# Kernel tuning notes

Measured on AMD Instinct MI355X. Metric: run time of the kernel, lower is better.

The kernel has to match this reference:

```python
import jax, jax.numpy as jnp
import numpy as np

VOCAB_SIZE = 250002
UNUSED_TOKEN_IDS = np.array([0, 2, 1, 3])  # cls, eos, pad, unk (XLM-R tokenizer)
EPS = 1e-12


def _l2norm(x):
    n = jnp.sqrt(jnp.sum(x * x, axis=-1, keepdims=True))
    return x / jnp.maximum(n, EPS)


def setup_inputs() -> dict:
    key = jax.random.key(0)
    k1, k2, k3, k4 = jax.random.split(key, 4)
    B, S, H = 16, 2048, 1024
    hidden_state = jax.random.normal(k1, (B, S, H), dtype=jnp.float32)
    attention_mask = jnp.ones((B, S), dtype=jnp.float32)
    input_ids = jax.random.randint(k2, (B, S), 0, VOCAB_SIZE, dtype=jnp.int64)
    sparse_W = jax.random.normal(k3, (H, 1), dtype=jnp.float32) * 0.02
    sparse_b = jnp.zeros((1,), dtype=jnp.float32)
    colbert_W = jax.random.normal(k4, (H, H), dtype=jnp.float32) * 0.02
    colbert_b = jnp.zeros((H,), dtype=jnp.float32)
    return {
        "hidden_state": hidden_state,
        "attention_mask": attention_mask,
        "input_ids": input_ids,
        "sparse_W": sparse_W,
        "sparse_b": sparse_b,
        "colbert_W": colbert_W,
        "colbert_b": colbert_b,
    }


def reference(hidden_state, attention_mask, input_ids, sparse_W, sparse_b, colbert_W, colbert_b):
    B, S, H = hidden_state.shape
    # dense vector: CLS token, L2-normalized
    dense_vecs = _l2norm(hidden_state[:, 0])  # (B, H)

    # sparse: relu(Linear(H,1)) per token, scatter into vocab, max over seq.
    # scatter into zeros(B,S,V) + max over dim=1 == per-batch scatter-max into (B,V)
    token_weights = jax.nn.relu(
        jnp.einsum("bsh,ho->bso", hidden_state, sparse_W) + sparse_b
    )[..., 0]  # (B, S)
    batch_idx = jnp.arange(B)[:, None]  # (B, 1)
    sparse_vecs = jnp.zeros((B, VOCAB_SIZE), dtype=token_weights.dtype)
    sparse_vecs = sparse_vecs.at[batch_idx, input_ids].max(token_weights)
    # zero out special tokens (cls/eos/pad/unk)
    sparse_vecs = sparse_vecs.at[:, jnp.asarray(UNUSED_TOKEN_IDS)].set(0.0)

    # colbert: Linear(H,H) on tokens 1:, masked, then L2-normalized
    colbert_vecs = jnp.einsum("bsh,hd->bsd", hidden_state[:, 1:], colbert_W) + colbert_b
    colbert_vecs = colbert_vecs * attention_mask[:, 1:, None]
    colbert_vecs = _l2norm(colbert_vecs)  # (B, S-1, H)

    return dense_vecs, sparse_vecs, colbert_vecs
```

## Files before the change

### kernel.cpp

```cpp
#include <hip/hip_runtime.h>
#include <hip/hip_bf16.h>

#define HDIM 1024
#define SEQ  2048
#define BATCH 16
#define VOCAB 250002
#define M_TOT (BATCH * SEQ)
#define DENSE_OFF 0
#define SPARSE_OFF (BATCH * HDIM)
#define COLBERT_OFF (SPARSE_OFF + BATCH * VOCAB)
#define COLBERT_ROWS (BATCH * (SEQ - 1))

typedef __attribute__((ext_vector_type(8))) short short8;
typedef __attribute__((ext_vector_type(4))) float f32x4;

static __device__ __forceinline__ unsigned short f2bf(float f) {
  union { float f; unsigned u; } v; v.f = f;
  unsigned r = v.u + 0x7fffu + ((v.u >> 16) & 1u);
  return (unsigned short)(r >> 16);
}

__global__ __launch_bounds__(256) void cast_sparse_kernel(
    const float* __restrict__ hidden,
    const float* __restrict__ sparse_W,
    const float* __restrict__ sparse_b,
    const int* __restrict__ input_ids,
    unsigned short* __restrict__ hidden_bf,
    float* __restrict__ sparse_out)
{
  const int token = blockIdx.x * 4 + (threadIdx.x >> 6);
  const int lane = threadIdx.x & 63;

  const float4* xr = (const float4*)(hidden + (size_t)token * HDIM);
  const float4* wr = (const float4*)sparse_W;
  ushort4* hb = (ushort4*)(hidden_bf + (size_t)token * HDIM);

  float dot = 0.0f;
#pragma unroll
  for (int i = 0; i < 4; i++) {
    const int idx = i * 64 + lane;
    float4 xv = xr[idx];
    float4 wv = wr[idx];
    dot = fmaf(xv.x, wv.x, dot);
    dot = fmaf(xv.y, wv.y, dot);
    dot = fmaf(xv.z, wv.z, dot);
    dot = fmaf(xv.w, wv.w, dot);
    ushort4 o;
    o.x = f2bf(xv.x); o.y = f2bf(xv.y); o.z = f2bf(xv.z); o.w = f2bf(xv.w);
    hb[idx] = o;
  }
#pragma unroll
  for (int off = 32; off; off >>= 1) dot += __shfl_down(dot, off);

  if (lane == 0) {
    float w = dot + sparse_b[0];
    if (w > 0.0f) {
      int id = input_ids[token];
      if (id > 3) {
        int b = token >> 11;
        atomicMax((int*)(sparse_out + (size_t)b * VOCAB + id), __float_as_int(w));
      }
    }
  }
}

__global__ __launch_bounds__(256) void dense_kernel(
    const float* __restrict__ hidden, float* __restrict__ out)
{
  const int b = blockIdx.x;
  const int t = threadIdx.x;
  const float4* x = (const float4*)(hidden + (size_t)b * SEQ * HDIM);
  float4 v = x[t];
  float ss = v.x * v.x + v.y * v.y + v.z * v.z + v.w * v.w;
#pragma unroll
  for (int off = 32; off; off >>= 1) ss += __shfl_down(ss, off);
  __shared__ float red[4];
  if ((t & 63) == 0) red[t >> 6] = ss;
  __syncthreads();
  float tot = red[0] + red[1] + red[2] + red[3];
  float inv = 1.0f / fmaxf(sqrtf(tot), 1e-12f);
  v.x *= inv; v.y *= inv; v.z *= inv; v.w *= inv;
  ((float4*)(out + (size_t)b * HDIM))[t] = v;
}

__global__ __launch_bounds__(256) void transpose_w_kernel(
    const float* __restrict__ W, unsigned short* __restrict__ Wt)
{
  __shared__ float tile[32][33];
  const int n0 = blockIdx.x * 32, k0 = blockIdx.y * 32;
  const int tx = threadIdx.x, ty = threadIdx.y;
#pragma unroll
  for (int i = ty; i < 32; i += 8)
    tile[i][tx] = W[(size_t)(k0 + i) * HDIM + n0 + tx];
  __syncthreads();
#pragma unroll
  for (int i = ty; i < 32; i += 8)
    Wt[(size_t)(n0 + i) * HDIM + k0 + tx] = f2bf(tile[tx][i]);
}

__global__ __launch_bounds__(256) void gemm_colbert_kernel(
    const unsigned short* __restrict__ Abf,
    const unsigned short* __restrict__ Btbf,
    const float* __restrict__ bias,
    float* __restrict__ out)
{
  __shared__ __attribute__((aligned(16))) unsigned short As[128 * 32];
  __shared__ __attribute__((aligned(16))) unsigned short Bs[128 * 32];

  const int t = threadIdx.x;
  const int wv = t >> 6, l = t & 63;
  const int nt = blockIdx.x & 7, mt = blockIdx.x >> 3;
  const int mBase = mt * 128, nBase = nt * 128;
  const int wm = wv >> 1, wn = wv & 1;
  const int q = l >> 4, ml = l & 15;

  f32x4 acc[4][4] = {};

  const int c0 = t;
  const int c1 = t + 256;
  const unsigned short* Ab = Abf + (size_t)mBase * HDIM;
  const unsigned short* Bb = Btbf + (size_t)nBase * HDIM;
  const size_t ga0 = (size_t)(c0 >> 2) * HDIM + (c0 & 3) * 8;
  const size_t ga1 = (size_t)(c1 >> 2) * HDIM + (c1 & 3) * 8;

  for (int k0 = 0; k0 < HDIM; k0 += 32) {
    __builtin_amdgcn_global_load_lds(
        (const __attribute__((address_space(1))) unsigned int*)(Ab + k0 + ga0),
        (__attribute__((address_space(3))) unsigned int*)(As + wv * 512), 16, 0, 0);
    __builtin_amdgcn_global_load_lds(
        (const __attribute__((address_space(1))) unsigned int*)(Ab + k0 + ga1),
        (__attribute__((address_space(3))) unsigned int*)(As + 2048 + wv * 512), 16, 0, 0);
    __builtin_amdgcn_global_load_lds(
        (const __attribute__((address_space(1))) unsigned int*)(Bb + k0 + ga0),
        (__attribute__((address_space(3))) unsigned int*)(Bs + wv * 512), 16, 0, 0);
    __builtin_amdgcn_global_load_lds(
        (const __attribute__((address_space(1))) unsigned int*)(Bb + k0 + ga1),
        (__attribute__((address_space(3))) unsigned int*)(Bs + 2048 + wv * 512), 16, 0, 0);
    __syncthreads();

    short8 af[4], bf[4];
#pragma unroll
    for (int i = 0; i < 4; i++) {
      af[i] = *(const short8*)(As + (wm * 64 + i * 16 + ml) * 32 + q * 8);
      bf[i] = *(const short8*)(Bs + (wn * 64 + i * 16 + ml) * 32 + q * 8);
    }
#pragma unroll
    for (int i = 0; i < 4; i++)
#pragma unroll
      for (int j = 0; j < 4; j++)
        acc[i][j] = __builtin_amdgcn_mfma_f32_16x16x32_bf16(af[i], bf[j], acc[i][j], 0, 0, 0);
    __syncthreads();
  }

#pragma unroll
  for (int j = 0; j < 4; j++) {
    const int gn = nBase + wn * 64 + j * 16 + ml;
    const float bv = bias[gn];
#pragma unroll
    for (int i = 0; i < 4; i++) {
#pragma unroll
      for (int r = 0; r < 4; r++) {
        const int gm = mBase + wm * 64 + i * 16 + q * 4 + r;
        const int s = gm & (SEQ - 1);
        if (s != 0) {
          const int b = gm >> 11;
          out[COLBERT_OFF + (size_t)(b * (SEQ - 1) + s - 1) * HDIM + gn] =
              acc[i][j][r] + bv;
        }
      }
    }
  }
}

__global__ __launch_bounds__(256) void colbert_norm_kernel(
    float* __restrict__ out, const float* __restrict__ mask)
{
  const int row = blockIdx.x;
  const int b = row / (SEQ - 1);
  const int s = row - b * (SEQ - 1) + 1;
  const float mval = mask[b * SEQ + s];

  float4* p = (float4*)(out + COLBERT_OFF + (size_t)row * HDIM);
  float4 v = p[threadIdx.x];
  v.x *= mval; v.y *= mval; v.z *= mval; v.w *= mval;
  float ss = v.x * v.x + v.y * v.y + v.z * v.z + v.w * v.w;
#pragma unroll
  for (int off = 32; off; off >>= 1) ss += __shfl_down(ss, off);
  __shared__ float red[4];
  if ((threadIdx.x & 63) == 0) red[threadIdx.x >> 6] = ss;
  __syncthreads();
  float tot = red[0] + red[1] + red[2] + red[3];
  float inv = 1.0f / fmaxf(sqrtf(tot), 1e-12f);
  v.x *= inv; v.y *= inv; v.z *= inv; v.w *= inv;
  p[threadIdx.x] = v;
}

extern "C" void kernel_launch(void* const* d_in, const int* in_sizes, int n_in,
                              void* d_out, int out_size, void* d_ws, size_t ws_size,
                              hipStream_t stream) {
  (void)in_sizes; (void)n_in; (void)out_size; (void)ws_size;
  const float* hidden = (const float*)d_in[0];
  const float* attn_mask = (const float*)d_in[1];
  const int* input_ids = (const int*)d_in[2];
  const float* sparse_W = (const float*)d_in[3];
  const float* sparse_b = (const float*)d_in[4];
  const float* colbert_W = (const float*)d_in[5];
  const float* colbert_b = (const float*)d_in[6];
  float* out = (float*)d_out;

  unsigned short* hidden_bf = (unsigned short*)d_ws;
  unsigned short* Wt = (unsigned short*)((char*)d_ws + (size_t)M_TOT * HDIM * 2);

  hipMemsetAsync(out + SPARSE_OFF, 0, (size_t)BATCH * VOCAB * sizeof(float), stream);

  cast_sparse_kernel<<<M_TOT / 4, 256, 0, stream>>>(
      hidden, sparse_W, sparse_b, input_ids, hidden_bf, out + SPARSE_OFF);
  transpose_w_kernel<<<dim3(32, 32), dim3(32, 8), 0, stream>>>(colbert_W, Wt);
  dense_kernel<<<BATCH, 256, 0, stream>>>(hidden, out);
  gemm_colbert_kernel<<<(M_TOT / 128) * (HDIM / 128), 256, 0, stream>>>(
      hidden_bf, Wt, colbert_b, out);
  colbert_norm_kernel<<<COLBERT_ROWS, 256, 0, stream>>>(out, attn_mask);
}
```

Before: 399.8 us.

## Swizzle GEMM LDS layout, remap tiles per XCD, use wave-per-row colbert norm

Remaps GEMM block indices so each XCD processes a contiguous band of M tiles, improving L2 reuse of A and B. Applies an XOR-style rotation to the 16-byte chunks written to and read from LDS to reduce bank conflicts on MFMA fragment loads. Rewrites the colbert normalization so one wavefront handles a full row, with shuffle-only reduction and no shared memory or barrier, folding the mask into the scale factor.

After: 382.5 us. 1.05x faster.

```diff
diff --git a/kernel.cpp b/kernel.cpp
--- a/kernel.cpp
+++ b/kernel.cpp
@@ -109,7 +109,11 @@
 
   const int t = threadIdx.x;
   const int wv = t >> 6, l = t & 63;
-  const int nt = blockIdx.x & 7, mt = blockIdx.x >> 3;
+
+  const int xcd = blockIdx.x & 7;
+  const int local = blockIdx.x >> 3;
+  const int mt = xcd * 32 + (local >> 3);
+  const int nt = local & 7;
   const int mBase = mt * 128, nBase = nt * 128;
   const int wm = wv >> 1, wn = wv & 1;
   const int q = l >> 4, ml = l & 15;
@@ -118,10 +122,12 @@
 
   const int c0 = t;
   const int c1 = t + 256;
+  const int r0 = c0 >> 2, r1 = c1 >> 2;
+  const size_t ga0 = (size_t)r0 * HDIM + (((c0 & 3) - (r0 >> 1)) & 3) * 8;
+  const size_t ga1 = (size_t)r1 * HDIM + (((c1 & 3) - (r1 >> 1)) & 3) * 8;
+
   const unsigned short* Ab = Abf + (size_t)mBase * HDIM;
   const unsigned short* Bb = Btbf + (size_t)nBase * HDIM;
-  const size_t ga0 = (size_t)(c0 >> 2) * HDIM + (c0 & 3) * 8;
-  const size_t ga1 = (size_t)(c1 >> 2) * HDIM + (c1 & 3) * 8;
 
   for (int k0 = 0; k0 < HDIM; k0 += 32) {
     __builtin_amdgcn_global_load_lds(
@@ -141,8 +147,10 @@
     short8 af[4], bf[4];
 #pragma unroll
     for (int i = 0; i < 4; i++) {
-      af[i] = *(const short8*)(As + (wm * 64 + i * 16 + ml) * 32 + q * 8);
-      bf[i] = *(const short8*)(Bs + (wn * 64 + i * 16 + ml) * 32 + q * 8);
+      const int ar = wm * 64 + i * 16 + ml;
+      const int br = wn * 64 + i * 16 + ml;
+      af[i] = *(const short8*)(As + ar * 32 + (((q + (ar >> 1)) & 3) * 8));
+      bf[i] = *(const short8*)(Bs + br * 32 + (((q + (br >> 1)) & 3) * 8));
     }
 #pragma unroll
     for (int i = 0; i < 4; i++)
@@ -175,24 +183,28 @@
 __global__ __launch_bounds__(256) void colbert_norm_kernel(
     float* __restrict__ out, const float* __restrict__ mask)
 {
-  const int row = blockIdx.x;
+  const int row = blockIdx.x * 4 + (threadIdx.x >> 6);
+  const int lane = threadIdx.x & 63;
   const int b = row / (SEQ - 1);
   const int s = row - b * (SEQ - 1) + 1;
   const float mval = mask[b * SEQ + s];
 
   float4* p = (float4*)(out + COLBERT_OFF + (size_t)row * HDIM);
-  float4 v = p[threadIdx.x];
-  v.x *= mval; v.y *= mval; v.z *= mval; v.w *= mval;
-  float ss = v.x * v.x + v.y * v.y + v.z * v.z + v.w * v.w;
-#pragma unroll
-  for (int off = 32; off; off >>= 1) ss += __shfl_down(ss, off);
-  __shared__ float red[4];
-  if ((threadIdx.x & 63) == 0) red[threadIdx.x >> 6] = ss;
-  __syncthreads();
-  float tot = red[0] + red[1] + red[2] + red[3];
-  float inv = 1.0f / fmaxf(sqrtf(tot), 1e-12f);
-  v.x *= inv; v.y *= inv; v.z *= inv; v.w *= inv;
-  p[threadIdx.x] = v;
+  float4 v[4];
+  float ss = 0.0f;
+#pragma unroll
+  for (int i = 0; i < 4; i++) {
+    v[i] = p[i * 64 + lane];
+    ss += v[i].x * v[i].x + v[i].y * v[i].y + v[i].z * v[i].z + v[i].w * v[i].w;
+  }
+#pragma unroll
+  for (int off = 32; off; off >>= 1) ss += __shfl_xor(ss, off);
+  const float inv = mval / fmaxf(fabsf(mval) * sqrtf(ss), 1e-12f);
+#pragma unroll
+  for (int i = 0; i < 4; i++) {
+    v[i].x *= inv; v[i].y *= inv; v[i].z *= inv; v[i].w *= inv;
+    p[i * 64 + lane] = v[i];
+  }
 }
 
 extern "C" void kernel_launch(void* const* d_in, const int* in_sizes, int n_in,
@@ -219,5 +231,5 @@
   dense_kernel<<<BATCH, 256, 0, stream>>>(hidden, out);
   gemm_colbert_kernel<<<(M_TOT / 128) * (HDIM / 128), 256, 0, stream>>>(
       hidden_bf, Wt, colbert_b, out);
-  colbert_norm_kernel<<<COLBERT_ROWS, 256, 0, stream>>>(out, attn_mask);
-}
+  colbert_norm_kernel<<<COLBERT_ROWS / 4, 256, 0, stream>>>(out, attn_mask);
+}
```
